# Performance work log

Measured on AMD Instinct MI355X. Metric: run time of the kernel, lower is better.

Reference implementation:

```python
import jax, jax.numpy as jnp
import numpy as np

N, E, B, IN, OUT = 100000, 1000000, 8, 64, 64


def gcn_conv(X, edge_index, edge_weight, W, b):
    """PyG GCNConv with add_self_loops=True, improved=False (self-loop weight 1)."""
    n = X.shape[0]
    row, col = edge_index[0], edge_index[1]
    loop = jnp.arange(n)
    row = jnp.concatenate([row, loop])
    col = jnp.concatenate([col, loop])
    ew = jnp.concatenate([edge_weight, jnp.ones((n,), X.dtype)])
    deg = jax.ops.segment_sum(ew, col, num_segments=n)
    dinv = jnp.where(deg > 0, jax.lax.rsqrt(deg), 0.0)
    norm = dinv[row] * ew * dinv[col]  # [E+N]
    xw = X @ W  # [N, OUT]
    msg = norm[:, None] * xw[row]  # gather
    out = jax.ops.segment_sum(msg, col, num_segments=n)  # scatter-add
    return out + b


def mean_pool(x, batch, num_graphs):
    s = jax.ops.segment_sum(x, batch, num_segments=num_graphs)
    cnt = jax.ops.segment_sum(jnp.ones((x.shape[0],), x.dtype), batch, num_segments=num_graphs)
    return s / jnp.maximum(cnt, 1.0)[:, None]


def setup_inputs() -> dict:
    key = jax.random.key(0)
    ks = jax.random.split(key, 16)
    inp = {
        "X": jax.random.normal(ks[0], (N, IN), jnp.float32),
        "edge_index": jax.random.randint(ks[1], (2, E), 0, N),
        "readout_batch": jnp.sort(jax.random.randint(ks[2], (N,), 0, B)),
        "edge_weight": jax.random.uniform(ks[3], (E,), jnp.float32),
        "H": jax.random.normal(ks[4], (B, OUT), jnp.float32),
    }
    sc = 1.0 / np.sqrt(IN)
    sl = 1.0 / np.sqrt(2 * OUT)
    for i, g in enumerate(["z", "r", "h"]):
        inp[f"W_{g}"] = jax.random.uniform(ks[5 + i], (IN, OUT), jnp.float32, -sc, sc)
        inp[f"b_{g}"] = jnp.zeros((OUT,), jnp.float32)
        inp[f"lin_{g}_W"] = jax.random.uniform(ks[8 + i], (2 * OUT, OUT), jnp.float32, -sl, sl)
        inp[f"lin_{g}_b"] = jax.random.uniform(ks[11 + i], (OUT,), jnp.float32, -sl, sl)
    return inp


def reference(X, edge_index, readout_batch, edge_weight, H,
              W_z, b_z, lin_z_W, lin_z_b,
              W_r, b_r, lin_r_W, lin_r_b,
              W_h, b_h, lin_h_W, lin_h_b):
    num_graphs = H.shape[0]

    def gate(W, b, linW, linb):
        t = gcn_conv(X, edge_index, edge_weight, W, b)
        t = mean_pool(t, readout_batch, num_graphs)  # [B, OUT]
        return jnp.concatenate([t, H], axis=1) @ linW + linb

    Z = jax.nn.sigmoid(gate(W_z, b_z, lin_z_W, lin_z_b))
    R = jax.nn.sigmoid(gate(W_r, b_r, lin_r_W, lin_r_b))  # computed but unused, as in source
    H_tilde = jnp.tanh(gate(W_h, b_h, lin_h_W, lin_h_b))
    H_new = Z * H + (1.0 - Z) * H_tilde
    return H_new
```

## Files before the change

kernel.cpp:

```cpp
#include <hip/hip_runtime.h>
#include <math.h>

#define N_NODES 100000
#define N_EDGES 1000000
#define NB 8
#define NBUCK 256
#define BROWS 392
#define CAP 6144
#define NPAIR 256
#define CHUNKC 3907
#define ITER 8


__global__ __launch_bounds__(512) void kInit(int* __restrict__ cursors) {
    const int t = threadIdx.x;
    const int b = (t < NBUCK) ? t : t - NBUCK;
    cursors[t * 16] = b * CAP;
}

__global__ __launch_bounds__(512) void kC_both(const int* __restrict__ row,
        const int* __restrict__ col, const float* __restrict__ ew,
        int* __restrict__ cursors, uint2* __restrict__ rowBin,
        uint2* __restrict__ colBin) {
    __shared__ int hist[NBUCK], base_[NBUCK], off[NBUCK];
    const int tid  = threadIdx.x;
    const int role = blockIdx.x & 1;
    const int cid  = blockIdx.x >> 1;
    const int* idxp = role ? col : row;
    int* cursor = cursors + role * NBUCK * 16;
    uint2* bin  = role ? colBin : rowBin;

    if (tid < NBUCK) hist[tid] = 0;
    __syncthreads();

    const int beg = cid * CHUNKC;
    const int end = min(N_EDGES, beg + CHUNKC);
    int ix[ITER]; float wv[ITER]; int ox[ITER];
    #pragma unroll
    for (int it = 0; it < ITER; ++it) {
        const int i = beg + it * 512 + tid;
        if (i < end) {
            ix[it] = idxp[i]; wv[it] = ew[i];
            atomicAdd(&hist[ix[it] / BROWS], 1);
        } else ix[it] = -1;
    }
    if (!role) {
        #pragma unroll
        for (int it = 0; it < ITER; ++it) {
            const int i = beg + it * 512 + tid;
            ox[it] = (i < end) ? col[i] : 0;
        }
    }
    __syncthreads();

    if (tid < NBUCK) {
        const int rnd = (hist[tid] + 7) & ~7;
        const int b = atomicAdd(&cursor[tid * 16], rnd);
        base_[tid] = b; off[tid] = b;
    }
    __syncthreads();

    #pragma unroll
    for (int it = 0; it < ITER; ++it) {
        if (ix[it] >= 0) {
            const int x = ix[it];
            const int kb = x / BROWS;
            const int xl = x - kb * BROWS;
            const int p = atomicAdd(&off[kb], 1);
            if (p < (kb + 1) * CAP) {
                const unsigned key = role ? (unsigned)xl
                                          : (unsigned)((ox[it] << 9) | xl);
                bin[p] = make_uint2(key, __float_as_uint(wv[it]));
            }
        }
    }
    __syncthreads();

    for (int b = tid; b < NBUCK; b += 512) {
        const int e = min(base_[b] + ((hist[b] + 7) & ~7), (b + 1) * CAP);
        for (int p = off[b]; p < e; ++p) bin[p] = make_uint2(0u, 0u);
    }
}

__global__ __launch_bounds__(512) void kD_degacc(const uint2* __restrict__ colBin,
        const int* __restrict__ cursors, const int* __restrict__ batch,
        uint2* __restrict__ db, float* __restrict__ cntT) {
    __shared__ float degsub[BROWS];
    __shared__ float cb[NB];
    const int tid = threadIdx.x;
    const int kb  = blockIdx.x;
    if (tid < BROWS) degsub[tid] = 0.f;
    if (tid < NB) cb[tid] = 0.f;
    __syncthreads();
    const int beg = kb * CAP;
    const int end = min(cursors[(NBUCK + kb) * 16], beg + CAP);
    for (int i = beg + tid; i < end; i += 512) {
        const uint2 v = colBin[i];
        atomicAdd(&degsub[v.x], __uint_as_float(v.y));
    }
    __syncthreads();
    if (tid < BROWS) {
        const int r = kb * BROWS + tid;
        if (r < N_NODES) {
            const float dv = rsqrtf(degsub[tid] + 1.0f);
            const int g = batch[r];
            db[r] = make_uint2(__float_as_uint(dv), (unsigned)g);
            atomicAdd(&cb[g], 1.0f);
        }
    }
    __syncthreads();
    if (tid < NB) cntT[kb * NB + tid] = cb[tid];
}

__global__ __launch_bounds__(512) void kD_bucket(const float* __restrict__ X,
        const uint2* __restrict__ rowBin, const int* __restrict__ cursors,
        const uint2* __restrict__ db, float* __restrict__ partial) {
    __shared__ float Ssub[BROWS * NB];
    __shared__ float red[512];
    const int tid = threadIdx.x;
    const int kb  = blockIdx.x;
    const int r0  = kb * BROWS;

    for (int i = tid; i < BROWS * NB; i += 512) Ssub[i] = 0.f;
    __syncthreads();

    const int beg = kb * CAP;
    const int end = min(cursors[kb * 16], beg + CAP);
    for (int i = beg + tid; i < end; i += 512) {
        const uint2 v = rowBin[i];
        const uint2 d = db[v.x >> 9];
        atomicAdd(&Ssub[((v.x & 511) << 3) | d.y],
                  __uint_as_float(d.x) * __uint_as_float(v.y));
    }
    if (tid < BROWS) {
        const int r = r0 + tid;
        if (r < N_NODES) {
            const uint2 d = db[r];
            atomicAdd(&Ssub[(tid << 3) | d.y], __uint_as_float(d.x));
        }
    }
    __syncthreads();

    const int k4  = tid & 15;
    const int rid = tid >> 4;
    float acc[8][4];
    #pragma unroll
    for (int g = 0; g < 8; ++g)
        #pragma unroll
        for (int c = 0; c < 4; ++c) acc[g][c] = 0.f;

    for (int it = 0; it < (BROWS + 31) / 32; ++it) {
        const int lr = it * 32 + rid;
        const int r  = r0 + lr;
        if (lr < BROWS && r < N_NODES) {
            const float dv = __uint_as_float(db[r].x);
            const float4 x  = *reinterpret_cast<const float4*>(X + (long)r * 64 + k4 * 4);
            float4 s0 = *reinterpret_cast<const float4*>(&Ssub[lr * 8]);
            float4 s1 = *reinterpret_cast<const float4*>(&Ssub[lr * 8 + 4]);
            const float sg[8] = {s0.x * dv, s0.y * dv, s0.z * dv, s0.w * dv,
                                 s1.x * dv, s1.y * dv, s1.z * dv, s1.w * dv};
            #pragma unroll
            for (int g = 0; g < 8; ++g) {
                acc[g][0] += sg[g] * x.x;
                acc[g][1] += sg[g] * x.y;
                acc[g][2] += sg[g] * x.z;
                acc[g][3] += sg[g] * x.w;
            }
        }
    }

    #pragma unroll
    for (int g = 0; g < 8; ++g)
        #pragma unroll
        for (int c = 0; c < 4; ++c) {
            float v = acc[g][c];
            v += __shfl_xor(v, 16);
            v += __shfl_xor(v, 32);
            acc[g][c] = v;
        }

    red[tid] = 0.f;
    __syncthreads();
    if ((tid & 48) == 0) {
        #pragma unroll
        for (int g = 0; g < 8; ++g)
            #pragma unroll
            for (int c = 0; c < 4; ++c)
                atomicAdd(&red[g * 64 + k4 * 4 + c], acc[g][c]);
    }
    __syncthreads();
    partial[(long)kb * 512 + tid] = red[tid];
}

__global__ __launch_bounds__(64) void k45_reduce(const float* __restrict__ partial,
        const float* __restrict__ cntT, float* __restrict__ Y, float* __restrict__ cnt) {
    const int bid = blockIdx.x;
    const int lane = threadIdx.x;
    if (bid < 512) {
        float s = 0.f;
        for (int b = lane; b < NBUCK; b += 64)
            s += partial[(long)b * 512 + bid];
        #pragma unroll
        for (int m = 1; m <= 32; m <<= 1) s += __shfl_xor(s, m);
        if (lane == 0) Y[bid] = s;
    } else {
        const int g = bid - 512;
        float s = 0.f;
        for (int kb = lane; kb < NBUCK; kb += 64)
            s += cntT[kb * NB + g];
        #pragma unroll
        for (int m = 1; m <= 32; m <<= 1) s += __shfl_xor(s, m);
        if (lane == 0) cnt[g] = fmaxf(s, 1.0f);
    }
}

__global__ __launch_bounds__(512) void kTail(const float* __restrict__ Y,
        const float* __restrict__ cnt, const float* __restrict__ H,
        const float* __restrict__ Wz, const float* __restrict__ bz,
        const float* __restrict__ lzW, const float* __restrict__ lzb,
        const float* __restrict__ Wh, const float* __restrict__ bh,
        const float* __restrict__ lhW, const float* __restrict__ lhb,
        float* __restrict__ out) {
    __shared__ float Ws[64 * 64];
    __shared__ float lWs[128 * 64];
    __shared__ float Ys[512], Hs[512], P[512], Gz[512];
    __shared__ float cnt_s[NB];
    const int t = threadIdx.x;
    const int g = t >> 6, j = t & 63;

    const float yv = Y[t];
    if (t < NB) cnt_s[t] = cnt[t];
    Hs[t] = H[t];
    {
        const float4* W4  = reinterpret_cast<const float4*>(Wz);
        const float4* lW4 = reinterpret_cast<const float4*>(lzW);
        float4* Ws4  = reinterpret_cast<float4*>(Ws);
        float4* lWs4 = reinterpret_cast<float4*>(lWs);
        #pragma unroll
        for (int i = 0; i < 2; ++i) Ws4[t + 512 * i] = W4[t + 512 * i];
        #pragma unroll
        for (int i = 0; i < 4; ++i) lWs4[t + 512 * i] = lW4[t + 512 * i];
    }
    __syncthreads();
    Ys[t] = yv / cnt_s[g];
    __syncthreads();

    float p = bz[j];
    #pragma unroll 8
    for (int k = 0; k < 64; ++k) p += Ys[g * 64 + k] * Ws[k * 64 + j];
    P[t] = p;
    __syncthreads();
    float az = lzb[j];
    #pragma unroll 8
    for (int k = 0; k < 64; ++k)
        az += P[g * 64 + k] * lWs[k * 64 + j] + Hs[g * 64 + k] * lWs[(64 + k) * 64 + j];
    Gz[t] = 1.f / (1.f + expf(-az));
    __syncthreads();

    {
        const float4* W4  = reinterpret_cast<const float4*>(Wh);
        const float4* lW4 = reinterpret_cast<const float4*>(lhW);
        float4* Ws4  = reinterpret_cast<float4*>(Ws);
        float4* lWs4 = reinterpret_cast<float4*>(lWs);
        #pragma unroll
        for (int i = 0; i < 2; ++i) Ws4[t + 512 * i] = W4[t + 512 * i];
        #pragma unroll
        for (int i = 0; i < 4; ++i) lWs4[t + 512 * i] = lW4[t + 512 * i];
    }
    __syncthreads();

    p = bh[j];
    #pragma unroll 8
    for (int k = 0; k < 64; ++k) p += Ys[g * 64 + k] * Ws[k * 64 + j];
    P[t] = p;
    __syncthreads();
    float ah = lhb[j];
    #pragma unroll 8
    for (int k = 0; k < 64; ++k)
        ah += P[g * 64 + k] * lWs[k * 64 + j] + Hs[g * 64 + k] * lWs[(64 + k) * 64 + j];
    const float Ht = tanhf(ah);

    out[t] = Gz[t] * Hs[t] + (1.f - Gz[t]) * Ht;
}

extern "C" void kernel_launch(void* const* d_in, const int* in_sizes, int n_in,
                              void* d_out, int out_size, void* d_ws, size_t ws_size,
                              hipStream_t stream) {
    (void)in_sizes; (void)n_in; (void)out_size; (void)ws_size;

    const float* X     = (const float*)d_in[0];
    const int*   ei    = (const int*)d_in[1];
    const int*   rowp  = ei;
    const int*   colp  = ei + N_EDGES;
    const int*   batch = (const int*)d_in[2];
    const float* ew    = (const float*)d_in[3];
    const float* H     = (const float*)d_in[4];
    const float* Wz  = (const float*)d_in[5];
    const float* bz  = (const float*)d_in[6];
    const float* lzW = (const float*)d_in[7];
    const float* lzb = (const float*)d_in[8];
    const float* Wh  = (const float*)d_in[13];
    const float* bh  = (const float*)d_in[14];
    const float* lhW = (const float*)d_in[15];
    const float* lhb = (const float*)d_in[16];
    float* out = (float*)d_out;

    const long NCAP = (long)NBUCK * CAP;
    int*   cursors = (int*)d_ws;
    float* cntT    = (float*)(cursors + 2 * NBUCK * 16);
    float* partial = cntT + NBUCK * NB;
    float* cnt     = partial + (long)NBUCK * 512;
    float* Yv      = cnt + 8;
    uint2* db      = (uint2*)(Yv + 512);
    uint2* rowBin  = db + N_NODES;
    uint2* colBin  = rowBin + NCAP;

    kInit<<<1, 512, 0, stream>>>(cursors);
    kC_both<<<2 * NPAIR, 512, 0, stream>>>(rowp, colp, ew, cursors, rowBin, colBin);
    kD_degacc<<<NBUCK, 512, 0, stream>>>(colBin, cursors, batch, db, cntT);
    kD_bucket<<<NBUCK, 512, 0, stream>>>(X, rowBin, cursors, db, partial);
    k45_reduce<<<520, 64, 0, stream>>>(partial, cntT, Yv, cnt);
    kTail<<<1, 512, 0, stream>>>(Yv, cnt, H, Wz, bz, lzW, lzb, Wh, bh, lhW, lhb, out);
}
```

Measured before the change: 73.20 us.

## Replace column binning with global degree atomics and stage row bins in LDS

Removes the separate column-bucket binning pass and the per-bucket degree kernel. Edge weights are now atomically added straight into a global degree array while the row-bucket pass runs. The row-binning kernel first scatters each chunk's edges into shared memory using a block-local prefix scan, then writes contiguous per-bucket runs to global memory for more coalesced stores. Graph node counts go into a global atomic accumulator, which shrinks the reduction kernel. The cost is a million scattered global float atomics and the loss of the zero padding to multiples of 8 in the row bins.

```diff
diff --git a/kernel.cpp b/kernel.cpp
--- a/kernel.cpp
+++ b/kernel.cpp
@@ -7,109 +7,100 @@
 #define NBUCK 256
 #define BROWS 392
 #define CAP 6144
-#define NPAIR 256
+#define NCHUNK 256
 #define CHUNKC 3907
 #define ITER 8
 
 
-__global__ __launch_bounds__(512) void kInit(int* __restrict__ cursors) {
-    const int t = threadIdx.x;
-    const int b = (t < NBUCK) ? t : t - NBUCK;
-    cursors[t * 16] = b * CAP;
-}
-
-__global__ __launch_bounds__(512) void kC_both(const int* __restrict__ row,
+__global__ __launch_bounds__(512) void kInit(int* __restrict__ cursors,
+        float* __restrict__ deg, float* __restrict__ cntG) {
+    const int t = blockIdx.x * 512 + threadIdx.x;
+    if (t < NBUCK) cursors[t * 16] = t * CAP;
+    if (t < NB) cntG[t] = 0.f;
+    for (int i = t; i < N_NODES; i += 256 * 512) deg[i] = 0.f;
+}
+
+__global__ __launch_bounds__(512) void kC(const int* __restrict__ row,
         const int* __restrict__ col, const float* __restrict__ ew,
         int* __restrict__ cursors, uint2* __restrict__ rowBin,
-        uint2* __restrict__ colBin) {
-    __shared__ int hist[NBUCK], base_[NBUCK], off[NBUCK];
-    const int tid  = threadIdx.x;
-    const int role = blockIdx.x & 1;
-    const int cid  = blockIdx.x >> 1;
-    const int* idxp = role ? col : row;
-    int* cursor = cursors + role * NBUCK * 16;
-    uint2* bin  = role ? colBin : rowBin;
+        float* __restrict__ deg) {
+    __shared__ uint2 sPay[CHUNKC];
+    __shared__ unsigned char sBkt[CHUNKC];
+    __shared__ int hist[NBUCK], scan[NBUCK], gbase[NBUCK], off[NBUCK];
+    const int tid = threadIdx.x;
+    const int beg = blockIdx.x * CHUNKC;
+    const int end = min(N_EDGES, beg + CHUNKC);
 
     if (tid < NBUCK) hist[tid] = 0;
     __syncthreads();
 
-    const int beg = cid * CHUNKC;
-    const int end = min(N_EDGES, beg + CHUNKC);
-    int ix[ITER]; float wv[ITER]; int ox[ITER];
+    int rx[ITER], cx[ITER]; float wv[ITER];
     #pragma unroll
     for (int it = 0; it < ITER; ++it) {
         const int i = beg + it * 512 + tid;
         if (i < end) {
-            ix[it] = idxp[i]; wv[it] = ew[i];
-            atomicAdd(&hist[ix[it] / BROWS], 1);
-        } else ix[it] = -1;
-    }
-    if (!role) {
-        #pragma unroll
-        for (int it = 0; it < ITER; ++it) {
-            const int i = beg + it * 512 + tid;
-            ox[it] = (i < end) ? col[i] : 0;
+            rx[it] = row[i]; cx[it] = col[i]; wv[it] = ew[i];
+            atomicAdd(&hist[rx[it] / BROWS], 1);
+            atomicAdd(&deg[cx[it]], wv[it]);
+        } else rx[it] = -1;
+    }
+    __syncthreads();
+
+    if (tid < NBUCK) scan[tid] = hist[tid];
+    __syncthreads();
+    for (int s = 1; s < NBUCK; s <<= 1) {
+        int v = 0;
+        if (tid < NBUCK && tid >= s) v = scan[tid - s];
+        __syncthreads();
+        if (tid < NBUCK) scan[tid] += v;
+        __syncthreads();
+    }
+
+    if (tid < NBUCK) {
+        const int lb = scan[tid] - hist[tid];
+        scan[tid] = lb;
+        off[tid] = lb;
+        gbase[tid] = atomicAdd(&cursors[tid * 16], hist[tid]);
+    }
+    __syncthreads();
+
+    #pragma unroll
+    for (int it = 0; it < ITER; ++it) {
+        if (rx[it] >= 0) {
+            const int kb = rx[it] / BROWS;
+            const int xl = rx[it] - kb * BROWS;
+            const int p = atomicAdd(&off[kb], 1);
+            sPay[p] = make_uint2((unsigned)((cx[it] << 9) | xl),
+                                 __float_as_uint(wv[it]));
+            sBkt[p] = (unsigned char)kb;
         }
     }
     __syncthreads();
 
-    if (tid < NBUCK) {
-        const int rnd = (hist[tid] + 7) & ~7;
-        const int b = atomicAdd(&cursor[tid * 16], rnd);
-        base_[tid] = b; off[tid] = b;
-    }
-    __syncthreads();
-
-    #pragma unroll
-    for (int it = 0; it < ITER; ++it) {
-        if (ix[it] >= 0) {
-            const int x = ix[it];
-            const int kb = x / BROWS;
-            const int xl = x - kb * BROWS;
-            const int p = atomicAdd(&off[kb], 1);
-            if (p < (kb + 1) * CAP) {
-                const unsigned key = role ? (unsigned)xl
-                                          : (unsigned)((ox[it] << 9) | xl);
-                bin[p] = make_uint2(key, __float_as_uint(wv[it]));
-            }
-        }
-    }
-    __syncthreads();
-
-    for (int b = tid; b < NBUCK; b += 512) {
-        const int e = min(base_[b] + ((hist[b] + 7) & ~7), (b + 1) * CAP);
-        for (int p = off[b]; p < e; ++p) bin[p] = make_uint2(0u, 0u);
-    }
-}
-
-__global__ __launch_bounds__(512) void kD_degacc(const uint2* __restrict__ colBin,
-        const int* __restrict__ cursors, const int* __restrict__ batch,
-        uint2* __restrict__ db, float* __restrict__ cntT) {
-    __shared__ float degsub[BROWS];
+    const int T = end - beg;
+    for (int j = tid; j < T; j += 512) {
+        const int b = sBkt[j];
+        const int dst = gbase[b] + (j - scan[b]);
+        if (dst < (b + 1) * CAP) rowBin[dst] = sPay[j];
+    }
+}
+
+__global__ __launch_bounds__(512) void kDb(const float* __restrict__ deg,
+        const int* __restrict__ batch, uint2* __restrict__ db,
+        float* __restrict__ cntG) {
     __shared__ float cb[NB];
     const int tid = threadIdx.x;
-    const int kb  = blockIdx.x;
-    if (tid < BROWS) degsub[tid] = 0.f;
     if (tid < NB) cb[tid] = 0.f;
     __syncthreads();
-    const int beg = kb * CAP;
-    const int end = min(cursors[(NBUCK + kb) * 16], beg + CAP);
-    for (int i = beg + tid; i < end; i += 512) {
-        const uint2 v = colBin[i];
-        atomicAdd(&degsub[v.x], __uint_as_float(v.y));
-    }
-    __syncthreads();
-    if (tid < BROWS) {
-        const int r = kb * BROWS + tid;
-        if (r < N_NODES) {
-            const float dv = rsqrtf(degsub[tid] + 1.0f);
-            const int g = batch[r];
-            db[r] = make_uint2(__float_as_uint(dv), (unsigned)g);
-            atomicAdd(&cb[g], 1.0f);
-        }
-    }
-    __syncthreads();
-    if (tid < NB) cntT[kb * NB + tid] = cb[tid];
+    const int i = blockIdx.x * 512 + tid;
+    if (i < N_NODES) {
+        const float dv = rsqrtf(deg[i] + 1.0f);
+        const int g = batch[i];
+        db[i] = make_uint2(__float_as_uint(dv), (unsigned)g);
+        atomicAdd(&cb[g], 1.0f);
+    }
+    __syncthreads();
+    if (tid < NB) atomicAdd(&cntG[tid], cb[tid]);
 }
 
 __global__ __launch_bounds__(512) void kD_bucket(const float* __restrict__ X,
@@ -193,25 +184,15 @@
 }
 
 __global__ __launch_bounds__(64) void k45_reduce(const float* __restrict__ partial,
-        const float* __restrict__ cntT, float* __restrict__ Y, float* __restrict__ cnt) {
+        float* __restrict__ Y) {
     const int bid = blockIdx.x;
     const int lane = threadIdx.x;
-    if (bid < 512) {
-        float s = 0.f;
-        for (int b = lane; b < NBUCK; b += 64)
-            s += partial[(long)b * 512 + bid];
-        #pragma unroll
-        for (int m = 1; m <= 32; m <<= 1) s += __shfl_xor(s, m);
-        if (lane == 0) Y[bid] = s;
-    } else {
-        const int g = bid - 512;
-        float s = 0.f;
-        for (int kb = lane; kb < NBUCK; kb += 64)
-            s += cntT[kb * NB + g];
-        #pragma unroll
-        for (int m = 1; m <= 32; m <<= 1) s += __shfl_xor(s, m);
-        if (lane == 0) cnt[g] = fmaxf(s, 1.0f);
-    }
+    float s = 0.f;
+    for (int b = lane; b < NBUCK; b += 64)
+        s += partial[(long)b * 512 + bid];
+    #pragma unroll
+    for (int m = 1; m <= 32; m <<= 1) s += __shfl_xor(s, m);
+    if (lane == 0) Y[bid] = s;
 }
 
 __global__ __launch_bounds__(512) void kTail(const float* __restrict__ Y,
@@ -229,7 +210,7 @@
     const int g = t >> 6, j = t & 63;
 
     const float yv = Y[t];
-    if (t < NB) cnt_s[t] = cnt[t];
+    if (t < NB) cnt_s[t] = fmaxf(cnt[t], 1.0f);
     Hs[t] = H[t];
     {
         const float4* W4  = reinterpret_cast<const float4*>(Wz);
@@ -305,20 +286,18 @@
     const float* lhb = (const float*)d_in[16];
     float* out = (float*)d_out;
 
-    const long NCAP = (long)NBUCK * CAP;
     int*   cursors = (int*)d_ws;
-    float* cntT    = (float*)(cursors + 2 * NBUCK * 16);
-    float* partial = cntT + NBUCK * NB;
-    float* cnt     = partial + (long)NBUCK * 512;
-    float* Yv      = cnt + 8;
-    uint2* db      = (uint2*)(Yv + 512);
+    float* cntG    = (float*)(cursors + NBUCK * 16);
+    float* partial = cntG + NB;
+    float* Yv      = partial + (long)NBUCK * 512;
+    float* deg     = Yv + 512;
+    uint2* db      = (uint2*)(deg + N_NODES);
     uint2* rowBin  = db + N_NODES;
-    uint2* colBin  = rowBin + NCAP;
-
-    kInit<<<1, 512, 0, stream>>>(cursors);
-    kC_both<<<2 * NPAIR, 512, 0, stream>>>(rowp, colp, ew, cursors, rowBin, colBin);
-    kD_degacc<<<NBUCK, 512, 0, stream>>>(colBin, cursors, batch, db, cntT);
+
+    kInit<<<256, 512, 0, stream>>>(cursors, deg, cntG);
+    kC<<<NCHUNK, 512, 0, stream>>>(rowp, colp, ew, cursors, rowBin, deg);
+    kDb<<<(N_NODES + 511) / 512, 512, 0, stream>>>(deg, batch, db, cntG);
     kD_bucket<<<NBUCK, 512, 0, stream>>>(X, rowBin, cursors, db, partial);
-    k45_reduce<<<520, 64, 0, stream>>>(partial, cntT, Yv, cnt);
-    kTail<<<1, 512, 0, stream>>>(Yv, cnt, H, Wz, bz, lzW, lzb, Wh, bh, lhW, lhb, out);
-}
+    k45_reduce<<<512, 64, 0, stream>>>(partial, Yv);
+    kTail<<<1, 512, 0, stream>>>(Yv, cntG, H, Wz, bz, lzW, lzb, Wh, bh, lhW, lhb, out);
+}
```

Measured after the change: 107.3 us. 1.47x slower.
